# Optimization experiments

Measured on AMD Instinct MI355X. Metric: run time of the kernel, lower is better.

## Reference

```python
import jax, jax.numpy as jnp
import numpy as np

N = 100_000; E = 3_200_000; F = 128; HID = 64; L = 4; H = 4; HD = 16; EMB = 64


def _ln(x, g, b):
    m = x.mean(-1, keepdims=True)
    v = ((x - m) ** 2).mean(-1, keepdims=True)
    return (x - m) / jnp.sqrt(v + 1e-5) * g + b


def _gelu(x):
    return jax.nn.gelu(x, approximate=False)


def _gat(h, src, dst, invalid, Wl, al, Wo):
    # Wl: (H, HID, HD), al: (H, 2*HD), Wo: (H*HD, HID)
    hh = jnp.einsum('nf,hfd->hnd', h, Wl)          # (H, N, HD)
    hs = hh[:, src]                                 # (H, E, HD) gather
    hd = hh[:, dst]                                 # (H, E, HD) gather
    e = jnp.einsum('hed,hd->he', hs, al[:, :HD]) + jnp.einsum('hed,hd->he', hd, al[:, HD:])
    e = jnp.where(e >= 0, e, 0.2 * e)               # LeakyReLU(0.2)
    e = jnp.where(invalid[None, :], -jnp.inf, e)
    seg_max = jax.vmap(lambda v: jax.ops.segment_max(v, dst, num_segments=N))(e)
    seg_max = jnp.where(jnp.isfinite(seg_max), seg_max, 0.0)  # empty segments -> 0 (matches include_self=False init 0)
    alpha = jnp.exp(jnp.minimum(e - seg_max[:, dst], 20.0))
    alpha = jnp.where(invalid[None, :], 0.0, alpha)
    asum = jax.vmap(lambda v: jax.ops.segment_sum(v, dst, num_segments=N))(alpha)
    an = alpha / (asum[:, dst] + 1e-8)
    msg = an[..., None] * hs                        # (H, E, HD)
    agg = jax.vmap(lambda m: jax.ops.segment_sum(m, dst, num_segments=N))(msg)  # (H, N, HD)
    return agg.transpose(1, 0, 2).reshape(N, H * HD) @ Wo


def setup_inputs() -> dict:
    key = jax.random.key(0)
    ks = jax.random.split(key, 20)
    rn = lambda k, shape, s: jax.random.normal(k, shape, jnp.float32) * s
    return {
        'node_features': jax.random.normal(ks[0], (N, F), jnp.float32),
        'edge_index': jax.random.randint(ks[1], (2, E), 0, N),
        'mask': jnp.ones((N,), bool),
        'ln_in_g': jnp.ones((F,), jnp.float32), 'ln_in_b': jnp.zeros((F,), jnp.float32),
        'W_in': rn(ks[2], (F, HID), 0.08), 'b_in': jnp.zeros((HID,), jnp.float32),
        'Wg': rn(ks[3], (L, H, HID, HD), 0.12),
        'attn': rn(ks[4], (L, H, 2 * HD), 0.2),
        'Wout': rn(ks[5], (L, H * HD, HID), 0.12),
        'norm_g': jnp.ones((L, HID), jnp.float32), 'norm_b': jnp.zeros((L, HID), jnp.float32),
        'We1': rn(ks[6], (HID, HID), 0.12), 'be1': jnp.zeros((HID,), jnp.float32),
        'We2': rn(ks[7], (HID, EMB), 0.12), 'be2': jnp.zeros((EMB,), jnp.float32),
        'Wrp': rn(ks[8], (HID, HID // 2), 0.12), 'brp': jnp.zeros((HID // 2,), jnp.float32),
        'Wro': rn(ks[9], (HID // 2, 1), 0.15), 'bro': jnp.zeros((1,), jnp.float32),
        'Wrs': rn(ks[10], (HID, 1), 0.12),
    }


def reference(node_features, edge_index, mask, ln_in_g, ln_in_b, W_in, b_in, Wg, attn, Wout,
              norm_g, norm_b, We1, be1, We2, be2, Wrp, brp, Wro, bro, Wrs):
    src, dst = edge_index[0], edge_index[1]
    invalid = ~mask[src]
    # input projection (dropout = eval identity)
    h = _gelu(_ln(node_features, ln_in_g, ln_in_b) @ W_in + b_in)
    for l in range(L):
        h = _ln(h + _gat(h, src, dst, invalid, Wg[l], attn[l], Wout[l]), norm_g[l], norm_b[l])
    hv = h  # mask is all-True so h[mask] == h (static shape)
    emb = jnp.tanh(_gelu(hv @ We1 + be1) @ We2 + be2)
    proj = _gelu(hv @ Wrp + brp)
    pred = (proj @ Wro + bro + hv @ Wrs)[:, 0]
    return pred, emb
```

## Files before the change

### kernel.cpp

```cpp
#include <hip/hip_runtime.h>
#include <hip/hip_bf16.h>
#include <hip/hip_fp16.h>
#include <math.h>

#define N_NODES 100000
#define E_EDGES 3200000
#define NQUADS  25000
#define LAYERS  4
#define NBKT    782
#define NB1     512
#define CHUNK1  6250

__device__ __forceinline__ float gelu_f(float x) {
    return 0.5f * x * (1.0f + erff(x * 0.70710678118654752f));
}
__device__ __forceinline__ float dot4(float4 a, float4 b) {
    return a.x * b.x + a.y * b.y + a.z * b.z + a.w * b.w;
}
__device__ __forceinline__ float4 fma4(float s, float4 w, float4 a) {
    a.x += s * w.x; a.y += s * w.y; a.z += s * w.z; a.w += s * w.w;
    return a;
}


__global__ __launch_bounds__(1024) void k_hist1(const int* __restrict__ dst,
        int* __restrict__ counts1) {
    __shared__ int hcnt[NBKT];
    int b = blockIdx.x;
    int lo = b * CHUNK1, hi = min(E_EDGES, lo + CHUNK1);
    for (int j = threadIdx.x; j < NBKT; j += 1024) hcnt[j] = 0;
    __syncthreads();
    for (int i = lo + (int)threadIdx.x; i < hi; i += 1024)
        atomicAdd(&hcnt[dst[i] >> 7], 1);
    __syncthreads();
    int* out = counts1 + (size_t)b * NBKT;
    for (int j = threadIdx.x; j < NBKT; j += 1024) out[j] = hcnt[j];
}

__global__ __launch_bounds__(NB1) void k_cscan(int* __restrict__ counts1,
        int* __restrict__ cdeg) {
    __shared__ int wsum[NB1 / 64];
    int bucket = blockIdx.x;
    int tid = threadIdx.x, lane = tid & 63, w = tid >> 6;
    int v = counts1[(size_t)tid * NBKT + bucket];
    int x = v;
    #pragma unroll
    for (int s = 1; s < 64; s <<= 1) {
        int t = __shfl_up(x, s, 64);
        if (lane >= s) x += t;
    }
    if (lane == 63) wsum[w] = x;
    __syncthreads();
    int woff = 0;
    for (int i = 0; i < w; ++i) woff += wsum[i];
    x += woff;
    counts1[(size_t)tid * NBKT + bucket] = x - v;
    if (tid == NB1 - 1) cdeg[bucket] = x;
}

__global__ __launch_bounds__(1024) void k_cstart(const int* __restrict__ cdeg,
        int* __restrict__ cstart, int* __restrict__ off) {
    __shared__ int wsum[16];
    int tid = threadIdx.x, lane = tid & 63, w = tid >> 6;
    int v = (tid < NBKT) ? cdeg[tid] : 0;
    int x = v;
    #pragma unroll
    for (int s = 1; s < 64; s <<= 1) {
        int t = __shfl_up(x, s, 64);
        if (lane >= s) x += t;
    }
    if (lane == 63) wsum[w] = x;
    __syncthreads();
    int woff = 0;
    for (int i = 0; i < w; ++i) woff += wsum[i];
    x += woff;
    if (tid < NBKT) cstart[tid] = x - v;
    if (tid == 0) off[N_NODES] = E_EDGES;
}

__global__ __launch_bounds__(1024) void k_scatter1(const int* __restrict__ src,
        const int* __restrict__ dst, const int* __restrict__ cstart,
        const int* __restrict__ counts1, int2* __restrict__ tmp) {
    __shared__ int hcnt[NBKT];
    int b = blockIdx.x;
    int lo = b * CHUNK1, hi = min(E_EDGES, lo + CHUNK1);
    const int* myoff = counts1 + (size_t)b * NBKT;
    for (int j = threadIdx.x; j < NBKT; j += 1024) hcnt[j] = 0;
    __syncthreads();
    for (int i = lo + (int)threadIdx.x; i < hi; i += 1024) {
        int s = src[i], d = dst[i];
        int bkt = d >> 7;
        int lr = atomicAdd(&hcnt[bkt], 1);
        int pos = cstart[bkt] + myoff[bkt] + lr;
        tmp[pos] = make_int2(s, d);
    }
}

__global__ __launch_bounds__(1024) void k_sort2(const int2* __restrict__ tmp,
        const int* __restrict__ cstart, const int* __restrict__ cdeg,
        int* __restrict__ off, int* __restrict__ csr_src) {
    __shared__ int hist[128];
    __shared__ int cur[128];
    __shared__ int wsum0;
    int k = blockIdx.x;
    int tid = threadIdx.x;
    int base = cstart[k], m = cdeg[k];
    if (tid < 128) hist[tid] = 0;
    __syncthreads();
    for (int i = tid; i < m; i += 1024)
        atomicAdd(&hist[tmp[base + i].y & 127], 1);
    __syncthreads();
    int v = 0, x = 0;
    if (tid < 128) { v = hist[tid]; x = v; }
    if (tid < 128) {
        int lane = tid & 63;
        #pragma unroll
        for (int s = 1; s < 64; s <<= 1) {
            int t = __shfl_up(x, s, 64);
            if (lane >= s) x += t;
        }
    }
    if (tid == 63) wsum0 = x;
    __syncthreads();
    if (tid < 128) {
        int excl = x - v + ((tid >= 64) ? wsum0 : 0);
        cur[tid] = excl;
        int node = k * 128 + tid;
        if (node < N_NODES) off[node] = base + excl;
    }
    __syncthreads();
    for (int i = tid; i < m; i += 1024) {
        int2 e = tmp[base + i];
        int r = atomicAdd(&cur[e.y & 127], 1);
        csr_src[base + r] = e.x;
    }
}


__global__ __launch_bounds__(256) void k_input(const float4* __restrict__ x4,
        const float4* __restrict__ g4, const float4* __restrict__ b4,
        const float4* __restrict__ Win4, const float4* __restrict__ bin4,
        float4* __restrict__ h4) {
    __shared__ float4 WL[128 * 16];
    __shared__ float4 gb[64];
    __shared__ float4 binL[16];
    __shared__ float4 hLw[4][4][33];
    for (int j = threadIdx.x; j < 2048; j += 256) WL[j] = Win4[j];
    if (threadIdx.x < 32) gb[threadIdx.x] = g4[threadIdx.x];
    else if (threadIdx.x < 64) gb[threadIdx.x] = b4[threadIdx.x - 32];
    else if (threadIdx.x < 80) binL[threadIdx.x - 64] = bin4[threadIdx.x - 64];
    __syncthreads();
    int lane = threadIdx.x & 63, wid = threadIdx.x >> 6;
    int c = lane & 15, n = lane >> 4;
    int gw = blockIdx.x * 4 + wid, nw = gridDim.x * 4;
    for (int quad = gw; quad < NQUADS; quad += nw) {
        int node = quad * 4 + n;
        float4 xa = x4[(size_t)node * 32 + c];
        float4 xb = x4[(size_t)node * 32 + 16 + c];
        float s = xa.x + xa.y + xa.z + xa.w + xb.x + xb.y + xb.z + xb.w;
        #pragma unroll
        for (int m = 8; m >= 1; m >>= 1) s += __shfl_xor(s, m, 64);
        float mean = s * (1.0f / 128.0f);
        float4 da = make_float4(xa.x - mean, xa.y - mean, xa.z - mean, xa.w - mean);
        float4 db = make_float4(xb.x - mean, xb.y - mean, xb.z - mean, xb.w - mean);
        float v = dot4(da, da) + dot4(db, db);
        #pragma unroll
        for (int m = 8; m >= 1; m >>= 1) v += __shfl_xor(v, m, 64);
        float rstd = rsqrtf(v * (1.0f / 128.0f) + 1e-5f);
        float4 ga = gb[c], gc = gb[c + 16], ba = gb[32 + c], bc = gb[48 + c];
        float4 na = make_float4(da.x * rstd * ga.x + ba.x, da.y * rstd * ga.y + ba.y,
                                da.z * rstd * ga.z + ba.z, da.w * rstd * ga.w + ba.w);
        float4 nb = make_float4(db.x * rstd * gc.x + bc.x, db.y * rstd * gc.y + bc.y,
                                db.z * rstd * gc.z + bc.z, db.w * rstd * gc.w + bc.w);
        hLw[wid][n][c] = na;
        hLw[wid][n][c + 16] = nb;
        float4 acc = binL[c];
        #pragma unroll 4
        for (int k4 = 0; k4 < 32; ++k4) {
            float4 xq = hLw[wid][n][k4];
            float4 w0 = WL[(k4 * 4 + 0) * 16 + c];
            float4 w1 = WL[(k4 * 4 + 1) * 16 + c];
            float4 w2 = WL[(k4 * 4 + 2) * 16 + c];
            float4 w3 = WL[(k4 * 4 + 3) * 16 + c];
            acc = fma4(xq.x, w0, acc);
            acc = fma4(xq.y, w1, acc);
            acc = fma4(xq.z, w2, acc);
            acc = fma4(xq.w, w3, acc);
        }
        float4 o = make_float4(gelu_f(acc.x), gelu_f(acc.y), gelu_f(acc.z), gelu_f(acc.w));
        h4[(size_t)quad * 64 + lane] = o;
    }
}


__global__ __launch_bounds__(256) void k_transform(const float4* __restrict__ h4,
        const float* __restrict__ Wg, const float4* __restrict__ al4,
        __half* __restrict__ hh, float* __restrict__ ssrc, float* __restrict__ sdst) {
    __shared__ float4 WL[64 * 16];
    __shared__ float4 aL[32];
    __shared__ float4 hLw[4][4][17];
    for (int j = threadIdx.x; j < 4096; j += 256) {
        int h_ = j >> 10, rem = j & 1023;
        int k = rem >> 4, d = rem & 15;
        ((float*)WL)[k * 64 + h_ * 16 + d] = Wg[j];
    }
    if (threadIdx.x < 32) aL[threadIdx.x] = al4[threadIdx.x];
    __syncthreads();
    int lane = threadIdx.x & 63, wid = threadIdx.x >> 6;
    int c = lane & 15, n = lane >> 4;
    int head = c >> 2, q = c & 3;
    float4 aA = aL[head * 8 + q];
    float4 aB = aL[head * 8 + 4 + q];
    int gw = blockIdx.x * 4 + wid, nw = gridDim.x * 4;
    for (int quad = gw; quad < NQUADS; quad += nw) {
        int node = quad * 4 + n;
        hLw[wid][n][c] = h4[(size_t)quad * 64 + lane];
        float4 acc = make_float4(0.f, 0.f, 0.f, 0.f);
        #pragma unroll 4
        for (int k4 = 0; k4 < 16; ++k4) {
            float4 xq = hLw[wid][n][k4];
            float4 w0 = WL[(k4 * 4 + 0) * 16 + c];
            float4 w1 = WL[(k4 * 4 + 1) * 16 + c];
            float4 w2 = WL[(k4 * 4 + 2) * 16 + c];
            float4 w3 = WL[(k4 * 4 + 3) * 16 + c];
            acc = fma4(xq.x, w0, acc);
            acc = fma4(xq.y, w1, acc);
            acc = fma4(xq.z, w2, acc);
            acc = fma4(xq.w, w3, acc);
        }
        __half2 lo = __floats2half2_rn(acc.x, acc.y);
        __half2 hi = __floats2half2_rn(acc.z, acc.w);
        uint2 pk = make_uint2(*(unsigned*)&lo, *(unsigned*)&hi);
        *(uint2*)(hh + (size_t)node * 64 + 4 * c) = pk;
        float t1 = dot4(acc, aA);
        float t2 = dot4(acc, aB);
        t1 += __shfl_xor(t1, 1, 64); t1 += __shfl_xor(t1, 2, 64);
        t2 += __shfl_xor(t2, 1, 64); t2 += __shfl_xor(t2, 2, 64);
        if (q == 0) {
            ssrc[node * 4 + head] = t1;
            sdst[node * 4 + head] = t2;
        }
    }
}


__device__ __forceinline__ float4 wmax4(float4 v) {
    #pragma unroll
    for (int m = 32; m >= 1; m >>= 1) {
        v.x = fmaxf(v.x, __shfl_xor(v.x, m, 64));
        v.y = fmaxf(v.y, __shfl_xor(v.y, m, 64));
        v.z = fmaxf(v.z, __shfl_xor(v.z, m, 64));
        v.w = fmaxf(v.w, __shfl_xor(v.w, m, 64));
    }
    return v;
}
__device__ __forceinline__ float4 wsum4(float4 v) {
    #pragma unroll
    for (int m = 32; m >= 1; m >>= 1) {
        v.x += __shfl_xor(v.x, m, 64);
        v.y += __shfl_xor(v.y, m, 64);
        v.z += __shfl_xor(v.z, m, 64);
        v.w += __shfl_xor(v.w, m, 64);
    }
    return v;
}
__device__ __forceinline__ float sel4(float4 v, int hd) {
    float r = v.x;
    if (hd == 1) r = v.y;
    if (hd == 2) r = v.z;
    if (hd == 3) r = v.w;
    return r;
}
__device__ __forceinline__ float4 leaky4(float4 s, float4 d) {
    float ex = s.x + d.x, ey = s.y + d.y, ez = s.z + d.z, ew = s.w + d.w;
    return make_float4((ex >= 0.f) ? ex : 0.2f * ex, (ey >= 0.f) ? ey : 0.2f * ey,
                       (ez >= 0.f) ? ez : 0.2f * ez, (ew >= 0.f) ? ew : 0.2f * ew);
}
__device__ __forceinline__ void acc8(float w, uint4 hv,
        float& a0, float& a1, float& a2, float& a3,
        float& a4, float& a5, float& a6, float& a7) {
    float2 f0 = __half22float2(*(__half2*)&hv.x);
    float2 f1 = __half22float2(*(__half2*)&hv.y);
    float2 f2 = __half22float2(*(__half2*)&hv.z);
    float2 f3 = __half22float2(*(__half2*)&hv.w);
    a0 += w * f0.x; a1 += w * f0.y; a2 += w * f1.x; a3 += w * f1.y;
    a4 += w * f2.x; a5 += w * f2.y; a6 += w * f3.x; a7 += w * f3.y;
}

__global__ __launch_bounds__(256) void k_edge(const int* __restrict__ off,
        const int* __restrict__ csr_src, const float4* __restrict__ ssrc4,
        const float4* __restrict__ sdst4, const __half* __restrict__ hh,
        float4* __restrict__ agg4, int n) {
    __shared__ float pbuf[4][64][4];
    int lane = threadIdx.x & 63, wid = threadIdx.x >> 6;
    int node = blockIdx.x * 4 + wid;
    if (node >= n) return;
    int sub = lane >> 3;
    int dp  = lane & 7;
    int hd2 = dp >> 1;
    float4 sd = sdst4[node];
    int s0 = off[node], s1 = off[node + 1];
    if (s0 == s1) {
        if (sub == 0) {
            float4 z = make_float4(0.f, 0.f, 0.f, 0.f);
            agg4[(size_t)node * 16 + dp * 2]     = z;
            agg4[(size_t)node * 16 + dp * 2 + 1] = z;
        }
        return;
    }
    float4 m4   = make_float4(-INFINITY, -INFINITY, -INFINITY, -INFINITY);
    float4 sum4 = make_float4(0.f, 0.f, 0.f, 0.f);
    float a0=0.f,a1=0.f,a2=0.f,a3=0.f,a4=0.f,a5=0.f,a6=0.f,a7=0.f;
    const __half* hrow = hh + dp * 8;
    int idx = s0 + lane;
    int sn = 0;
    float4 e4 = make_float4(-INFINITY, -INFINITY, -INFINITY, -INFINITY);
    if (idx < s1) {
        sn = csr_src[idx];
        e4 = leaky4(ssrc4[sn], sd);
    }
    for (int base = s0; base < s1; base += 64) {
        int cnt = min(64, s1 - base);
        int snc = sn;
        float4 e4c = e4;
        int nidx = base + 64 + lane;
        sn = 0;
        e4 = make_float4(-INFINITY, -INFINITY, -INFINITY, -INFINITY);
        if (nidx < s1) {
            sn = csr_src[nidx];
            e4 = leaky4(ssrc4[sn], sd);
        }
        float4 cm = wmax4(e4c);
        float4 mn = make_float4(fmaxf(m4.x, cm.x), fmaxf(m4.y, cm.y),
                                fmaxf(m4.z, cm.z), fmaxf(m4.w, cm.w));
        float4 scv = make_float4(__expf(m4.x - mn.x), __expf(m4.y - mn.y),
                                 __expf(m4.z - mn.z), __expf(m4.w - mn.w));
        float4 p4 = make_float4(__expf(e4c.x - mn.x), __expf(e4c.y - mn.y),
                                __expf(e4c.z - mn.z), __expf(e4c.w - mn.w));
        float4 sp = wsum4(p4);
        sum4.x = sum4.x * scv.x + sp.x;
        sum4.y = sum4.y * scv.y + sp.y;
        sum4.z = sum4.z * scv.z + sp.z;
        sum4.w = sum4.w * scv.w + sp.w;
        m4 = mn;
        *(float4*)&pbuf[wid][lane][0] = p4;
        float scm = sel4(scv, hd2);
        a0*=scm; a1*=scm; a2*=scm; a3*=scm; a4*=scm; a5*=scm; a6*=scm; a7*=scm;
        int cnt8 = (cnt + 7) & ~7;
        int j = 0;
        for (; j + 32 <= cnt8; j += 32) {
            int eA = j + sub, eB = j + 8 + sub, eC = j + 16 + sub, eD = j + 24 + sub;
            int sA = __shfl(snc, eA, 64);
            int sB = __shfl(snc, eB, 64);
            int sC = __shfl(snc, eC, 64);
            int sD = __shfl(snc, eD, 64);
            uint4 hA = *(const uint4*)(hrow + (size_t)sA * 64);
            uint4 hB = *(const uint4*)(hrow + (size_t)sB * 64);
            uint4 hC = *(const uint4*)(hrow + (size_t)sC * 64);
            uint4 hD = *(const uint4*)(hrow + (size_t)sD * 64);
            float wA = pbuf[wid][eA][hd2];
            float wB = pbuf[wid][eB][hd2];
            float wC = pbuf[wid][eC][hd2];
            float wD = pbuf[wid][eD][hd2];
            acc8(wA, hA, a0,a1,a2,a3,a4,a5,a6,a7);
            acc8(wB, hB, a0,a1,a2,a3,a4,a5,a6,a7);
            acc8(wC, hC, a0,a1,a2,a3,a4,a5,a6,a7);
            acc8(wD, hD, a0,a1,a2,a3,a4,a5,a6,a7);
        }
        for (; j < cnt8; j += 8) {
            int eA = j + sub;
            int sA = __shfl(snc, eA, 64);
            float wA = pbuf[wid][eA][hd2];
            uint4 hA = *(const uint4*)(hrow + (size_t)sA * 64);
            acc8(wA, hA, a0,a1,a2,a3,a4,a5,a6,a7);
        }
    }
    #pragma unroll
    for (int m = 8; m <= 32; m <<= 1) {
        a0 += __shfl_xor(a0, m, 64); a1 += __shfl_xor(a1, m, 64);
        a2 += __shfl_xor(a2, m, 64); a3 += __shfl_xor(a3, m, 64);
        a4 += __shfl_xor(a4, m, 64); a5 += __shfl_xor(a5, m, 64);
        a6 += __shfl_xor(a6, m, 64); a7 += __shfl_xor(a7, m, 64);
    }
    float inv = 1.0f / (sel4(sum4, hd2) + 1e-8f);
    if (sub == 0) {
        agg4[(size_t)node * 16 + dp * 2]     = make_float4(a0*inv, a1*inv, a2*inv, a3*inv);
        agg4[(size_t)node * 16 + dp * 2 + 1] = make_float4(a4*inv, a5*inv, a6*inv, a7*inv);
    }
}


__global__ __launch_bounds__(256) void k_out_tr(const float4* __restrict__ agg4,
        const float4* __restrict__ Wout4, float4* __restrict__ h4,
        const float4* __restrict__ ng4, const float4* __restrict__ nb4_,
        const float* __restrict__ Wg, const float4* __restrict__ al4,
        __half* __restrict__ hh, float* __restrict__ ssrc, float* __restrict__ sdst) {
    __shared__ float4 WL[64 * 16];
    __shared__ float4 WG[64 * 16];
    __shared__ float4 gnb[32];
    __shared__ float4 aL[32];
    __shared__ float4 hLw[4][4][17];
    for (int j = threadIdx.x; j < 1024; j += 256) WL[j] = Wout4[j];
    for (int j = threadIdx.x; j < 4096; j += 256) {
        int h_ = j >> 10, rem = j & 1023;
        int k = rem >> 4, d = rem & 15;
        ((float*)WG)[k * 64 + h_ * 16 + d] = Wg[j];
    }
    if (threadIdx.x < 16) gnb[threadIdx.x] = ng4[threadIdx.x];
    else if (threadIdx.x < 32) gnb[threadIdx.x] = nb4_[threadIdx.x - 16];
    else if (threadIdx.x < 64) aL[threadIdx.x - 32] = al4[threadIdx.x - 32];
    __syncthreads();
    int lane = threadIdx.x & 63, wid = threadIdx.x >> 6;
    int c = lane & 15, n = lane >> 4;
    int head = c >> 2, q = c & 3;
    float4 gg = gnb[c], bb = gnb[16 + c];
    float4 aA = aL[head * 8 + q];
    float4 aB = aL[head * 8 + 4 + q];
    int gw = blockIdx.x * 4 + wid, nw = gridDim.x * 4;
    for (int quad = gw; quad < NQUADS; quad += nw) {
        int node = quad * 4 + n;
        hLw[wid][n][c] = agg4[(size_t)quad * 64 + lane];
        float4 acc = make_float4(0.f, 0.f, 0.f, 0.f);
        #pragma unroll 4
        for (int k4 = 0; k4 < 16; ++k4) {
            float4 xq = hLw[wid][n][k4];
            float4 w0 = WL[(k4 * 4 + 0) * 16 + c];
            float4 w1 = WL[(k4 * 4 + 1) * 16 + c];
            float4 w2 = WL[(k4 * 4 + 2) * 16 + c];
            float4 w3 = WL[(k4 * 4 + 3) * 16 + c];
            acc = fma4(xq.x, w0, acc);
            acc = fma4(xq.y, w1, acc);
            acc = fma4(xq.z, w2, acc);
            acc = fma4(xq.w, w3, acc);
        }
        float4 hv = h4[(size_t)quad * 64 + lane];
        float4 r = make_float4(acc.x + hv.x, acc.y + hv.y, acc.z + hv.z, acc.w + hv.w);
        float s = r.x + r.y + r.z + r.w;
        #pragma unroll
        for (int m = 8; m >= 1; m >>= 1) s += __shfl_xor(s, m, 64);
        float mean = s * (1.f / 64.f);
        float4 d = make_float4(r.x - mean, r.y - mean, r.z - mean, r.w - mean);
        float v = dot4(d, d);
        #pragma unroll
        for (int m = 8; m >= 1; m >>= 1) v += __shfl_xor(v, m, 64);
        float rstd = rsqrtf(v * (1.f / 64.f) + 1e-5f);
        float4 o = make_float4(d.x * rstd * gg.x + bb.x, d.y * rstd * gg.y + bb.y,
                               d.z * rstd * gg.z + bb.z, d.w * rstd * gg.w + bb.w);
        h4[(size_t)quad * 64 + lane] = o;
        hLw[wid][n][c] = o;
        float4 acc2 = make_float4(0.f, 0.f, 0.f, 0.f);
        #pragma unroll 4
        for (int k4 = 0; k4 < 16; ++k4) {
            float4 xq = hLw[wid][n][k4];
            float4 w0 = WG[(k4 * 4 + 0) * 16 + c];
            float4 w1 = WG[(k4 * 4 + 1) * 16 + c];
            float4 w2 = WG[(k4 * 4 + 2) * 16 + c];
            float4 w3 = WG[(k4 * 4 + 3) * 16 + c];
            acc2 = fma4(xq.x, w0, acc2);
            acc2 = fma4(xq.y, w1, acc2);
            acc2 = fma4(xq.z, w2, acc2);
            acc2 = fma4(xq.w, w3, acc2);
        }
        __half2 lo = __floats2half2_rn(acc2.x, acc2.y);
        __half2 hi = __floats2half2_rn(acc2.z, acc2.w);
        uint2 pk = make_uint2(*(unsigned*)&lo, *(unsigned*)&hi);
        *(uint2*)(hh + (size_t)node * 64 + 4 * c) = pk;
        float t1 = dot4(acc2, aA);
        float t2 = dot4(acc2, aB);
        t1 += __shfl_xor(t1, 1, 64); t1 += __shfl_xor(t1, 2, 64);
        t2 += __shfl_xor(t2, 1, 64); t2 += __shfl_xor(t2, 2, 64);
        if (q == 0) {
            ssrc[node * 4 + head] = t1;
            sdst[node * 4 + head] = t2;
        }
    }
}


__global__ __launch_bounds__(256) void k_out(const float4* __restrict__ agg4,
        const float4* __restrict__ Wout4, float4* __restrict__ h4,
        const float4* __restrict__ ng4, const float4* __restrict__ nb4_) {
    __shared__ float4 WL[64 * 16];
    __shared__ float4 gnb[32];
    __shared__ float4 hLw[4][4][17];
    for (int j = threadIdx.x; j < 1024; j += 256) WL[j] = Wout4[j];
    if (threadIdx.x < 16) gnb[threadIdx.x] = ng4[threadIdx.x];
    else if (threadIdx.x < 32) gnb[threadIdx.x] = nb4_[threadIdx.x - 16];
    __syncthreads();
    int lane = threadIdx.x & 63, wid = threadIdx.x >> 6;
    int c = lane & 15, n = lane >> 4;
    float4 gg = gnb[c], bb = gnb[16 + c];
    int gw = blockIdx.x * 4 + wid, nw = gridDim.x * 4;
    for (int quad = gw; quad < NQUADS; quad += nw) {
        hLw[wid][n][c] = agg4[(size_t)quad * 64 + lane];
        float4 acc = make_float4(0.f, 0.f, 0.f, 0.f);
        #pragma unroll 4
        for (int k4 = 0; k4 < 16; ++k4) {
            float4 xq = hLw[wid][n][k4];
            float4 w0 = WL[(k4 * 4 + 0) * 16 + c];
            float4 w1 = WL[(k4 * 4 + 1) * 16 + c];
            float4 w2 = WL[(k4 * 4 + 2) * 16 + c];
            float4 w3 = WL[(k4 * 4 + 3) * 16 + c];
            acc = fma4(xq.x, w0, acc);
            acc = fma4(xq.y, w1, acc);
            acc = fma4(xq.z, w2, acc);
            acc = fma4(xq.w, w3, acc);
        }
        float4 hv = h4[(size_t)quad * 64 + lane];
        float4 r = make_float4(acc.x + hv.x, acc.y + hv.y, acc.z + hv.z, acc.w + hv.w);
        float s = r.x + r.y + r.z + r.w;
        #pragma unroll
        for (int m = 8; m >= 1; m >>= 1) s += __shfl_xor(s, m, 64);
        float mean = s * (1.f / 64.f);
        float4 d = make_float4(r.x - mean, r.y - mean, r.z - mean, r.w - mean);
        float v = dot4(d, d);
        #pragma unroll
        for (int m = 8; m >= 1; m >>= 1) v += __shfl_xor(v, m, 64);
        float rstd = rsqrtf(v * (1.f / 64.f) + 1e-5f);
        float4 o = make_float4(d.x * rstd * gg.x + bb.x, d.y * rstd * gg.y + bb.y,
                               d.z * rstd * gg.z + bb.z, d.w * rstd * gg.w + bb.w);
        h4[(size_t)quad * 64 + lane] = o;
    }
}


__global__ __launch_bounds__(256) void k_final(const float4* __restrict__ h4,
        const float4* __restrict__ We1_4, const float4* __restrict__ be1_4,
        const float4* __restrict__ We2_4, const float4* __restrict__ be2_4,
        const float4* __restrict__ Wrp_4, const float4* __restrict__ brp_4,
        const float4* __restrict__ Wro_4, const float* __restrict__ bro,
        const float4* __restrict__ Wrs_4,
        float* __restrict__ pred, float4* __restrict__ emb4) {
    __shared__ float4 W1L[64 * 16], W2L[64 * 16], WPL[64 * 8];
    __shared__ float4 be1L[16], be2L[16], brpL[8], wroL[8], wrsL[16];
    __shared__ float broL;
    __shared__ float4 hLw[4][4][17], uLw[4][4][17];
    for (int j = threadIdx.x; j < 1024; j += 256) { W1L[j] = We1_4[j]; W2L[j] = We2_4[j]; }
    for (int j = threadIdx.x; j < 512; j += 256) WPL[j] = Wrp_4[j];
    if (threadIdx.x < 16) be1L[threadIdx.x] = be1_4[threadIdx.x];
    else if (threadIdx.x < 32) be2L[threadIdx.x - 16] = be2_4[threadIdx.x - 16];
    else if (threadIdx.x < 40) brpL[threadIdx.x - 32] = brp_4[threadIdx.x - 32];
    else if (threadIdx.x < 48) wroL[threadIdx.x - 40] = Wro_4[threadIdx.x - 40];
    else if (threadIdx.x < 64) wrsL[threadIdx.x - 48] = Wrs_4[threadIdx.x - 48];
    if (threadIdx.x == 64) broL = bro[0];
    __syncthreads();
    int lane = threadIdx.x & 63, wid = threadIdx.x >> 6;
    int c = lane & 15, n = lane >> 4;
    int gw = blockIdx.x * 4 + wid, nw = gridDim.x * 4;
    for (int quad = gw; quad < NQUADS; quad += nw) {
        float4 hv = h4[(size_t)quad * 64 + lane];
        hLw[wid][n][c] = hv;
        float4 acc = be1L[c];
        #pragma unroll 4
        for (int k4 = 0; k4 < 16; ++k4) {
            float4 xq = hLw[wid][n][k4];
            float4 w0 = W1L[(k4 * 4 + 0) * 16 + c];
            float4 w1 = W1L[(k4 * 4 + 1) * 16 + c];
            float4 w2 = W1L[(k4 * 4 + 2) * 16 + c];
            float4 w3 = W1L[(k4 * 4 + 3) * 16 + c];
            acc = fma4(xq.x, w0, acc);
            acc = fma4(xq.y, w1, acc);
            acc = fma4(xq.z, w2, acc);
            acc = fma4(xq.w, w3, acc);
        }
        float4 u = make_float4(gelu_f(acc.x), gelu_f(acc.y), gelu_f(acc.z), gelu_f(acc.w));
        uLw[wid][n][c] = u;
        float4 acc2 = be2L[c];
        #pragma unroll 4
        for (int k4 = 0; k4 < 16; ++k4) {
            float4 xq = uLw[wid][n][k4];
            float4 w0 = W2L[(k4 * 4 + 0) * 16 + c];
            float4 w1 = W2L[(k4 * 4 + 1) * 16 + c];
            float4 w2 = W2L[(k4 * 4 + 2) * 16 + c];
            float4 w3 = W2L[(k4 * 4 + 3) * 16 + c];
            acc2 = fma4(xq.x, w0, acc2);
            acc2 = fma4(xq.y, w1, acc2);
            acc2 = fma4(xq.z, w2, acc2);
            acc2 = fma4(xq.w, w3, acc2);
        }
        float4 e = make_float4(tanhf(acc2.x), tanhf(acc2.y), tanhf(acc2.z), tanhf(acc2.w));
        emb4[(size_t)quad * 64 + lane] = e;
        float contrib = dot4(hv, wrsL[c]);
        if (c < 8) {
            float4 a3 = brpL[c];
            #pragma unroll 4
            for (int k4 = 0; k4 < 16; ++k4) {
                float4 xq = hLw[wid][n][k4];
                float4 w0 = WPL[(k4 * 4 + 0) * 8 + c];
                float4 w1 = WPL[(k4 * 4 + 1) * 8 + c];
                float4 w2 = WPL[(k4 * 4 + 2) * 8 + c];
                float4 w3 = WPL[(k4 * 4 + 3) * 8 + c];
                a3 = fma4(xq.x, w0, a3);
                a3 = fma4(xq.y, w1, a3);
                a3 = fma4(xq.z, w2, a3);
                a3 = fma4(xq.w, w3, a3);
            }
            float4 p = make_float4(gelu_f(a3.x), gelu_f(a3.y), gelu_f(a3.z), gelu_f(a3.w));
            contrib += dot4(p, wroL[c]);
        }
        #pragma unroll
        for (int m = 8; m >= 1; m >>= 1) contrib += __shfl_xor(contrib, m, 64);
        if (c == 0) pred[quad * 4 + n] = contrib + broL;
    }
}


extern "C" void kernel_launch(void* const* d_in, const int* in_sizes, int n_in,
                              void* d_out, int out_size, void* d_ws, size_t ws_size,
                              hipStream_t stream) {
    const float* node_features = (const float*)d_in[0];
    const int*   edge_index    = (const int*)d_in[1];
    const float* ln_in_g = (const float*)d_in[3];
    const float* ln_in_b = (const float*)d_in[4];
    const float* W_in    = (const float*)d_in[5];
    const float* b_in    = (const float*)d_in[6];
    const float* Wg      = (const float*)d_in[7];
    const float* attn    = (const float*)d_in[8];
    const float* Wout    = (const float*)d_in[9];
    const float* norm_g  = (const float*)d_in[10];
    const float* norm_b  = (const float*)d_in[11];
    const float* We1     = (const float*)d_in[12];
    const float* be1     = (const float*)d_in[13];
    const float* We2     = (const float*)d_in[14];
    const float* be2     = (const float*)d_in[15];
    const float* Wrp     = (const float*)d_in[16];
    const float* brp     = (const float*)d_in[17];
    const float* Wro     = (const float*)d_in[18];
    const float* bro     = (const float*)d_in[19];
    const float* Wrs     = (const float*)d_in[20];

    const int* src = edge_index;
    const int* dst = edge_index + E_EDGES;

    char* ws = (char*)d_ws;
    size_t o = 0;
    auto alloc = [&](size_t bytes) {
        void* p = ws + o;
        o += (bytes + 255) & ~(size_t)255;
        return p;
    };
    int*    off     = (int*)alloc((size_t)(N_NODES + 1) * 4);
    int*    csr_src = (int*)alloc((size_t)E_EDGES * 4);
    float*  h       = (float*)alloc((size_t)N_NODES * 64 * 4);
    __half* hh      = (__half*)alloc((size_t)N_NODES * 64 * 2);
    float*  agg     = (float*)alloc((size_t)N_NODES * 64 * 4);
    float*  ssrc    = (float*)alloc((size_t)N_NODES * 4 * 4);
    float*  sdst    = (float*)alloc((size_t)N_NODES * 4 * 4);
    int*    counts1 = (int*)h;
    int*    cdeg    = counts1 + (size_t)NB1 * NBKT;
    int*    cstart  = cdeg + 1024;
    int2*   tmp     = (int2*)agg;

    float* pred = (float*)d_out;
    float* emb  = (float*)d_out + N_NODES;

    k_hist1<<<NB1, 1024, 0, stream>>>(dst, counts1);
    k_cscan<<<NBKT, NB1, 0, stream>>>(counts1, cdeg);
    k_cstart<<<1, 1024, 0, stream>>>(cdeg, cstart, off);
    k_scatter1<<<NB1, 1024, 0, stream>>>(src, dst, cstart, counts1, tmp);
    k_sort2<<<NBKT, 1024, 0, stream>>>(tmp, cstart, cdeg, off, csr_src);

    k_input<<<768, 256, 0, stream>>>((const float4*)node_features, (const float4*)ln_in_g,
                                     (const float4*)ln_in_b, (const float4*)W_in,
                                     (const float4*)b_in, (float4*)h);
    k_transform<<<1024, 256, 0, stream>>>((const float4*)h, Wg, (const float4*)attn,
                                          hh, ssrc, sdst);
    for (int l = 0; l < LAYERS; ++l) {
        k_edge<<<NQUADS, 256, 0, stream>>>(off, csr_src, (const float4*)ssrc,
                                           (const float4*)sdst, hh, (float4*)agg, N_NODES);
        if (l < LAYERS - 1) {
            k_out_tr<<<1024, 256, 0, stream>>>((const float4*)agg,
                    (const float4*)(Wout + l * 4096), (float4*)h,
                    (const float4*)(norm_g + l * 64), (const float4*)(norm_b + l * 64),
                    Wg + (l + 1) * 4096, (const float4*)(attn + (l + 1) * 128),
                    hh, ssrc, sdst);
        } else {
            k_out<<<1024, 256, 0, stream>>>((const float4*)agg,
                    (const float4*)(Wout + l * 4096), (float4*)h,
                    (const float4*)(norm_g + l * 64), (const float4*)(norm_b + l * 64));
        }
    }
    k_final<<<768, 256, 0, stream>>>((const float4*)h, (const float4*)We1, (const float4*)be1,
                                     (const float4*)We2, (const float4*)be2,
                                     (const float4*)Wrp, (const float4*)brp,
                                     (const float4*)Wro, bro, (const float4*)Wrs,
                                     pred, (float4*)emb);
}
```

Before: 777.6 us.

## Split edge aggregation per head with head-major feature layout

Stores transformed node features and attention scores in head-major layout and launches the edge kernel with one block per (head, node-quad), each wave handling a single head. This simplifies the online softmax to scalar per-lane work and spreads edges over lane pairs, which is meant to cut shuffle and per-head select overhead. In exchange, the CSR indices and offsets are read four times, and each feature gather becomes a 32-byte row segment instead of a 128-byte row.

New measurement: 1.227 ms. +57.8%, slower.

```diff
diff --git a/kernel.cpp b/kernel.cpp
--- a/kernel.cpp
+++ b/kernel.cpp
@@ -231,51 +231,19 @@
         __half2 lo = __floats2half2_rn(acc.x, acc.y);
         __half2 hi = __floats2half2_rn(acc.z, acc.w);
         uint2 pk = make_uint2(*(unsigned*)&lo, *(unsigned*)&hi);
-        *(uint2*)(hh + (size_t)node * 64 + 4 * c) = pk;
+        *(uint2*)(hh + ((size_t)head * N_NODES + node) * 16 + 4 * q) = pk;
         float t1 = dot4(acc, aA);
         float t2 = dot4(acc, aB);
         t1 += __shfl_xor(t1, 1, 64); t1 += __shfl_xor(t1, 2, 64);
         t2 += __shfl_xor(t2, 1, 64); t2 += __shfl_xor(t2, 2, 64);
         if (q == 0) {
-            ssrc[node * 4 + head] = t1;
-            sdst[node * 4 + head] = t2;
-        }
-    }
-}
-
-
-__device__ __forceinline__ float4 wmax4(float4 v) {
-    #pragma unroll
-    for (int m = 32; m >= 1; m >>= 1) {
-        v.x = fmaxf(v.x, __shfl_xor(v.x, m, 64));
-        v.y = fmaxf(v.y, __shfl_xor(v.y, m, 64));
-        v.z = fmaxf(v.z, __shfl_xor(v.z, m, 64));
-        v.w = fmaxf(v.w, __shfl_xor(v.w, m, 64));
-    }
-    return v;
-}
-__device__ __forceinline__ float4 wsum4(float4 v) {
-    #pragma unroll
-    for (int m = 32; m >= 1; m >>= 1) {
-        v.x += __shfl_xor(v.x, m, 64);
-        v.y += __shfl_xor(v.y, m, 64);
-        v.z += __shfl_xor(v.z, m, 64);
-        v.w += __shfl_xor(v.w, m, 64);
-    }
-    return v;
-}
-__device__ __forceinline__ float sel4(float4 v, int hd) {
-    float r = v.x;
-    if (hd == 1) r = v.y;
-    if (hd == 2) r = v.z;
-    if (hd == 3) r = v.w;
-    return r;
-}
-__device__ __forceinline__ float4 leaky4(float4 s, float4 d) {
-    float ex = s.x + d.x, ey = s.y + d.y, ez = s.z + d.z, ew = s.w + d.w;
-    return make_float4((ex >= 0.f) ? ex : 0.2f * ex, (ey >= 0.f) ? ey : 0.2f * ey,
-                       (ez >= 0.f) ? ez : 0.2f * ez, (ew >= 0.f) ? ew : 0.2f * ew);
-}
+            ssrc[(size_t)head * N_NODES + node] = t1;
+            sdst[(size_t)head * N_NODES + node] = t2;
+        }
+    }
+}
+
+
 __device__ __forceinline__ void acc8(float w, uint4 hv,
         float& a0, float& a1, float& a2, float& a3,
         float& a4, float& a5, float& a6, float& a7) {
@@ -288,104 +256,77 @@
 }
 
 __global__ __launch_bounds__(256) void k_edge(const int* __restrict__ off,
-        const int* __restrict__ csr_src, const float4* __restrict__ ssrc4,
-        const float4* __restrict__ sdst4, const __half* __restrict__ hh,
-        float4* __restrict__ agg4, int n) {
-    __shared__ float pbuf[4][64][4];
+        const int* __restrict__ csr_src, const float* __restrict__ ssrc,
+        const float* __restrict__ sdst, const __half* __restrict__ hh,
+        float* __restrict__ agg, int n) {
+    __shared__ float pbuf[4][64];
     int lane = threadIdx.x & 63, wid = threadIdx.x >> 6;
-    int node = blockIdx.x * 4 + wid;
-    if (node >= n) return;
-    int sub = lane >> 3;
-    int dp  = lane & 7;
-    int hd2 = dp >> 1;
-    float4 sd = sdst4[node];
+    int head = blockIdx.x / NQUADS;
+    int quad = blockIdx.x - head * NQUADS;
+    int node = quad * 4 + wid;
+    const float* ssrc_h = ssrc + (size_t)head * N_NODES;
+    const __half* hh_h  = hh + (size_t)head * N_NODES * 16;
+    float sd = sdst[(size_t)head * N_NODES + node];
     int s0 = off[node], s1 = off[node + 1];
-    if (s0 == s1) {
-        if (sub == 0) {
-            float4 z = make_float4(0.f, 0.f, 0.f, 0.f);
-            agg4[(size_t)node * 16 + dp * 2]     = z;
-            agg4[(size_t)node * 16 + dp * 2 + 1] = z;
-        }
-        return;
-    }
-    float4 m4   = make_float4(-INFINITY, -INFINITY, -INFINITY, -INFINITY);
-    float4 sum4 = make_float4(0.f, 0.f, 0.f, 0.f);
+    int sub = lane >> 1, half = lane & 1;
+    float m = -INFINITY, ssum = 0.f;
     float a0=0.f,a1=0.f,a2=0.f,a3=0.f,a4=0.f,a5=0.f,a6=0.f,a7=0.f;
-    const __half* hrow = hh + dp * 8;
+    const __half* hrow = hh_h + half * 8;
     int idx = s0 + lane;
     int sn = 0;
-    float4 e4 = make_float4(-INFINITY, -INFINITY, -INFINITY, -INFINITY);
+    float e = -INFINITY;
     if (idx < s1) {
         sn = csr_src[idx];
-        e4 = leaky4(ssrc4[sn], sd);
+        float t = ssrc_h[sn] + sd;
+        e = (t >= 0.f) ? t : 0.2f * t;
     }
     for (int base = s0; base < s1; base += 64) {
         int cnt = min(64, s1 - base);
         int snc = sn;
-        float4 e4c = e4;
+        float ec = e;
         int nidx = base + 64 + lane;
-        sn = 0;
-        e4 = make_float4(-INFINITY, -INFINITY, -INFINITY, -INFINITY);
+        sn = 0; e = -INFINITY;
         if (nidx < s1) {
             sn = csr_src[nidx];
-            e4 = leaky4(ssrc4[sn], sd);
-        }
-        float4 cm = wmax4(e4c);
-        float4 mn = make_float4(fmaxf(m4.x, cm.x), fmaxf(m4.y, cm.y),
-                                fmaxf(m4.z, cm.z), fmaxf(m4.w, cm.w));
-        float4 scv = make_float4(__expf(m4.x - mn.x), __expf(m4.y - mn.y),
-                                 __expf(m4.z - mn.z), __expf(m4.w - mn.w));
-        float4 p4 = make_float4(__expf(e4c.x - mn.x), __expf(e4c.y - mn.y),
-                                __expf(e4c.z - mn.z), __expf(e4c.w - mn.w));
-        float4 sp = wsum4(p4);
-        sum4.x = sum4.x * scv.x + sp.x;
-        sum4.y = sum4.y * scv.y + sp.y;
-        sum4.z = sum4.z * scv.z + sp.z;
-        sum4.w = sum4.w * scv.w + sp.w;
-        m4 = mn;
-        *(float4*)&pbuf[wid][lane][0] = p4;
-        float scm = sel4(scv, hd2);
-        a0*=scm; a1*=scm; a2*=scm; a3*=scm; a4*=scm; a5*=scm; a6*=scm; a7*=scm;
-        int cnt8 = (cnt + 7) & ~7;
-        int j = 0;
-        for (; j + 32 <= cnt8; j += 32) {
-            int eA = j + sub, eB = j + 8 + sub, eC = j + 16 + sub, eD = j + 24 + sub;
-            int sA = __shfl(snc, eA, 64);
-            int sB = __shfl(snc, eB, 64);
-            int sC = __shfl(snc, eC, 64);
-            int sD = __shfl(snc, eD, 64);
-            uint4 hA = *(const uint4*)(hrow + (size_t)sA * 64);
-            uint4 hB = *(const uint4*)(hrow + (size_t)sB * 64);
-            uint4 hC = *(const uint4*)(hrow + (size_t)sC * 64);
-            uint4 hD = *(const uint4*)(hrow + (size_t)sD * 64);
-            float wA = pbuf[wid][eA][hd2];
-            float wB = pbuf[wid][eB][hd2];
-            float wC = pbuf[wid][eC][hd2];
-            float wD = pbuf[wid][eD][hd2];
-            acc8(wA, hA, a0,a1,a2,a3,a4,a5,a6,a7);
+            float t = ssrc_h[sn] + sd;
+            e = (t >= 0.f) ? t : 0.2f * t;
+        }
+        float cm = ec;
+        #pragma unroll
+        for (int s = 32; s >= 1; s >>= 1) cm = fmaxf(cm, __shfl_xor(cm, s, 64));
+        float mn = fmaxf(m, cm);
+        float sc = __expf(m - mn);
+        float p = __expf(ec - mn);
+        pbuf[wid][lane] = p;
+        float sp = p;
+        #pragma unroll
+        for (int s = 32; s >= 1; s >>= 1) sp += __shfl_xor(sp, s, 64);
+        ssum = ssum * sc + sp;
+        m = mn;
+        a0*=sc; a1*=sc; a2*=sc; a3*=sc; a4*=sc; a5*=sc; a6*=sc; a7*=sc;
+        int sA = __shfl(snc, sub, 64);
+        float wA = pbuf[wid][sub];
+        uint4 hA = *(const uint4*)(hrow + (size_t)sA * 16);
+        acc8(wA, hA, a0,a1,a2,a3,a4,a5,a6,a7);
+        if (cnt > 32) {
+            int sB = __shfl(snc, 32 + sub, 64);
+            float wB = pbuf[wid][32 + sub];
+            uint4 hB = *(const uint4*)(hrow + (size_t)sB * 16);
             acc8(wB, hB, a0,a1,a2,a3,a4,a5,a6,a7);
-            acc8(wC, hC, a0,a1,a2,a3,a4,a5,a6,a7);
-            acc8(wD, hD, a0,a1,a2,a3,a4,a5,a6,a7);
-        }
-        for (; j < cnt8; j += 8) {
-            int eA = j + sub;
-            int sA = __shfl(snc, eA, 64);
-            float wA = pbuf[wid][eA][hd2];
-            uint4 hA = *(const uint4*)(hrow + (size_t)sA * 64);
-            acc8(wA, hA, a0,a1,a2,a3,a4,a5,a6,a7);
         }
     }
     #pragma unroll
-    for (int m = 8; m <= 32; m <<= 1) {
-        a0 += __shfl_xor(a0, m, 64); a1 += __shfl_xor(a1, m, 64);
-        a2 += __shfl_xor(a2, m, 64); a3 += __shfl_xor(a3, m, 64);
-        a4 += __shfl_xor(a4, m, 64); a5 += __shfl_xor(a5, m, 64);
-        a6 += __shfl_xor(a6, m, 64); a7 += __shfl_xor(a7, m, 64);
-    }
-    float inv = 1.0f / (sel4(sum4, hd2) + 1e-8f);
+    for (int s = 2; s <= 32; s <<= 1) {
+        a0 += __shfl_xor(a0, s, 64); a1 += __shfl_xor(a1, s, 64);
+        a2 += __shfl_xor(a2, s, 64); a3 += __shfl_xor(a3, s, 64);
+        a4 += __shfl_xor(a4, s, 64); a5 += __shfl_xor(a5, s, 64);
+        a6 += __shfl_xor(a6, s, 64); a7 += __shfl_xor(a7, s, 64);
+    }
+    float inv = 1.0f / (ssum + 1e-8f);
     if (sub == 0) {
-        agg4[(size_t)node * 16 + dp * 2]     = make_float4(a0*inv, a1*inv, a2*inv, a3*inv);
-        agg4[(size_t)node * 16 + dp * 2 + 1] = make_float4(a4*inv, a5*inv, a6*inv, a7*inv);
+        float* out = agg + (size_t)node * 64 + head * 16 + half * 8;
+        *(float4*)out       = make_float4(a0*inv, a1*inv, a2*inv, a3*inv);
+        *(float4*)(out + 4) = make_float4(a4*inv, a5*inv, a6*inv, a7*inv);
     }
 }
 
@@ -464,14 +405,14 @@
         __half2 lo = __floats2half2_rn(acc2.x, acc2.y);
         __half2 hi = __floats2half2_rn(acc2.z, acc2.w);
         uint2 pk = make_uint2(*(unsigned*)&lo, *(unsigned*)&hi);
-        *(uint2*)(hh + (size_t)node * 64 + 4 * c) = pk;
+        *(uint2*)(hh + ((size_t)head * N_NODES + node) * 16 + 4 * q) = pk;
         float t1 = dot4(acc2, aA);
         float t2 = dot4(acc2, aB);
         t1 += __shfl_xor(t1, 1, 64); t1 += __shfl_xor(t1, 2, 64);
         t2 += __shfl_xor(t2, 1, 64); t2 += __shfl_xor(t2, 2, 64);
         if (q == 0) {
-            ssrc[node * 4 + head] = t1;
-            sdst[node * 4 + head] = t2;
+            ssrc[(size_t)head * N_NODES + node] = t1;
+            sdst[(size_t)head * N_NODES + node] = t2;
         }
     }
 }
@@ -666,8 +607,8 @@
     k_transform<<<1024, 256, 0, stream>>>((const float4*)h, Wg, (const float4*)attn,
                                           hh, ssrc, sdst);
     for (int l = 0; l < LAYERS; ++l) {
-        k_edge<<<NQUADS, 256, 0, stream>>>(off, csr_src, (const float4*)ssrc,
-                                           (const float4*)sdst, hh, (float4*)agg, N_NODES);
+        k_edge<<<4 * NQUADS, 256, 0, stream>>>(off, csr_src, ssrc, sdst, hh,
+                                               agg, N_NODES);
         if (l < LAYERS - 1) {
             k_out_tr<<<1024, 256, 0, stream>>>((const float4*)agg,
                     (const float4*)(Wout + l * 4096), (float4*)h,
```
